# Optimization experiments

Measured on AMD Instinct MI355X. Metric: run time of the kernel, lower is better.

The kernel has to match this reference:

```python
import jax, jax.numpy as jnp
import numpy as np
from jax import lax

C, K, EMB = 10, 32, 32
B, H, W = 32, 128, 128
DIRS = ((-1, 0), (1, 0), (0, -1), (0, 1))  # up, down, left, right


def _shift(x, dh, dw):
    # shift (B,H,W,...) by (dh,dw) with zero fill; x[b,h,w] <- x[b,h+dh,w+dw]
    pad = [(0, 0), (max(dh, 0), max(-dh, 0)), (max(dw, 0), max(-dw, 0))] + [(0, 0)] * (x.ndim - 3)
    xp = jnp.pad(x, pad)
    h0, w0 = max(-dh, 0), max(-dw, 0)
    return lax.dynamic_slice_in_dim(lax.dynamic_slice_in_dim(xp, h0, x.shape[1], 1), w0, x.shape[2], 2)


def conv(x, w, b):
    y = lax.conv_general_dilated(x, w, (1, 1), 'SAME',
                                 dimension_numbers=('NHWC', 'HWIO', 'NHWC'))
    return y + b


def small_cnn(x, w1, b1, w2, b2, w3, b3):
    x = jax.nn.relu(conv(x, w1, b1))
    x = jax.nn.relu(conv(x, w2, b2))
    return conv(x, w3, b3)


def neighbor_affinity(phi, tau=0.5):
    # phi: (B,H,W,D) -> w: (B,H,W,4) Gaussian feature affinity to 4 neighbors
    ones = jnp.ones(phi.shape[:3] + (1,), phi.dtype)
    ws = []
    for dh, dw in DIRS:
        nb = _shift(phi, dh, dw)
        valid = _shift(ones, dh, dw)[..., 0]
        d2 = jnp.sum((phi - nb) ** 2, axis=-1)
        ws.append(jnp.exp(-d2 / tau) * valid)
    return jnp.stack(ws, axis=-1)


def init_seeds_soft(Bv, Hv, Wv, Kv, dtype=jnp.float32):
    # K seeds on a gh x gw grid; soft assignment by squared distance
    gh = 4
    gw = Kv // gh
    sh = (jnp.arange(gh, dtype=dtype) + 0.5) * (Hv / gh)
    sw = (jnp.arange(gw, dtype=dtype) + 0.5) * (Wv / gw)
    seed_h = jnp.repeat(sh, gw)  # (K,)
    seed_w = jnp.tile(sw, gh)    # (K,)
    hh = jnp.arange(Hv, dtype=dtype)[:, None, None]
    ww = jnp.arange(Wv, dtype=dtype)[None, :, None]
    d2 = (hh - seed_h) ** 2 + (ww - seed_w) ** 2  # (H,W,K)
    sigma2 = (Hv / gh) * (Wv / gw)
    A = jax.nn.softmax(-d2 / sigma2, axis=-1)
    return jnp.broadcast_to(A[None], (Bv, Hv, Wv, Kv))


def soft_message_pass(A, w, beta=2.0):
    # aggregate neighbor assignments weighted by affinity, renormalize over K
    agg = jnp.zeros_like(A)
    for d, (dh, dw) in enumerate(DIRS):
        agg = agg + w[..., d:d + 1] * _shift(A, dh, dw)
    return jax.nn.softmax(beta * agg, axis=-1)


def soft_pool_features(G, A):
    # G:(B,H,W,C), A:(B,H,W,K) -> T:(B,K,1+2+C+4)
    Bv, Hv, Wv, Cv = G.shape
    eps = 1e-6
    mass = jnp.sum(A, axis=(1, 2)) + eps                      # (B,K)
    hh = (jnp.arange(Hv, dtype=G.dtype) + 0.5) / Hv
    ww = (jnp.arange(Wv, dtype=G.dtype) + 0.5) / Wv
    h_c = jnp.einsum('bhwk,h->bk', A, hh) / mass
    w_c = jnp.einsum('bhwk,w->bk', A, ww) / mass
    col = jnp.einsum('bhwk,bhwc->bkc', A, G) / mass[..., None]
    h2 = jnp.einsum('bhwk,h->bk', A, hh ** 2) / mass
    w2 = jnp.einsum('bhwk,w->bk', A, ww ** 2) / mass
    h_sd = jnp.sqrt(jax.nn.relu(h2 - h_c ** 2) + eps)
    w_sd = jnp.sqrt(jax.nn.relu(w2 - w_c ** 2) + eps)
    size = (mass / (Hv * Wv))[..., None]                      # (B,K,1)
    cen = jnp.stack([h_c, w_c], axis=-1)                      # (B,K,2)
    bbox = jnp.stack([h_c - h_sd, h_c + h_sd, w_c - w_sd, w_c + w_sd], axis=-1)
    return jnp.concatenate([size, cen, col, bbox], axis=-1)


def setup_inputs() -> dict:
    key = jax.random.key(0)
    ks = jax.random.split(key, 4)
    X = jax.random.randint(ks[0], (B, H, W), 0, C)
    w1 = jax.random.normal(ks[1], (3, 3, C, 32), jnp.float32) * (1.0 / np.sqrt(9 * C))
    w2 = jax.random.normal(ks[2], (3, 3, 32, 32), jnp.float32) * (1.0 / np.sqrt(9 * 32))
    w3 = jax.random.normal(ks[3], (1, 1, 32, EMB), jnp.float32) * (1.0 / np.sqrt(32))
    return {'X': X, 'w1': w1, 'b1': jnp.zeros((32,), jnp.float32),
            'w2': w2, 'b2': jnp.zeros((32,), jnp.float32),
            'w3': w3, 'b3': jnp.zeros((EMB,), jnp.float32)}


def reference(X, w1, b1, w2, b2, w3, b3):
    G = jax.nn.one_hot(X, C, dtype=jnp.float32)              # (B,H,W,C)
    phi = small_cnn(G, w1, b1, w2, b2, w3, b3)               # (B,H,W,EMB)
    w = neighbor_affinity(phi)                               # (B,H,W,4)
    A = init_seeds_soft(G.shape[0], G.shape[1], G.shape[2], K, G.dtype)
    for _ in range(8):
        A = soft_message_pass(A, w, beta=2.0)
    T = soft_pool_features(G, A)
    return A, T
```

## Files before the change

### kernel.cpp

```cpp
#include <hip/hip_runtime.h>
#include <math.h>

#define HD 128
#define WD 128
#define BB 32
#define KK 32
#define NPIX (BB*HD*WD)
#define PLANE ((size_t)NPIX*8)

typedef _Float16 f16;
typedef __attribute__((ext_vector_type(8))) _Float16 f16x8;
typedef __attribute__((ext_vector_type(4))) _Float16 f16x4;
typedef __attribute__((ext_vector_type(4))) float f32x4;

__device__ __forceinline__ int swz(int row, int g){
  return row*64 + (((g + (row >> 1)) & 3) << 4);
}

__device__ __forceinline__ float xexp2(float x){
#if __has_builtin(__builtin_amdgcn_exp2f)
  return __builtin_amdgcn_exp2f(x);
#else
  return exp2f(x);
#endif
}
__device__ __forceinline__ float xrcp(float x){
#if __has_builtin(__builtin_amdgcn_rcpf)
  return __builtin_amdgcn_rcpf(x);
#else
  return 1.f/x;
#endif
}
__device__ __forceinline__ f16x8 bc8(f16 x){
  f16x8 v;
  #pragma unroll
  for (int j = 0; j < 8; j++) v[j] = x;
  return v;
}

#define WSCALE 2.8853900817779268f

__global__ __launch_bounds__(512, 2) void cnn_kernel(
    const int* __restrict__ X,
    const float* __restrict__ w1, const float* __restrict__ b1,
    const float* __restrict__ w2, const float* __restrict__ b2,
    const float* __restrict__ w3, const float* __restrict__ b3,
    f16* __restrict__ phi)
{
  __shared__ f16 sW1f[9*11*40];
  __shared__ int   sX[20*36];
  __shared__ float sB2[32], sB3[32];
  __shared__ f16 x1[612*32];
  __shared__ f16 w2t[9*32*32];
  __shared__ f16 w3t[32*32];

  const int tid = threadIdx.x;
  const int img = blockIdx.z;
  const int bh0 = blockIdx.y * 16;
  const int bw0 = blockIdx.x * 32;

  for (int i = tid; i < 9*11*32; i += 512) {
    int tap = i / 352, c = (i % 352) >> 5, oc = i & 31;
    float v = (c < 10) ? w1[tap*320 + c*32 + oc] : 0.f;
    if (tap == 4 && c < 10) v += b1[oc];
    sW1f[(tap*11 + c)*40 + oc] = (f16)v;
  }
  for (int i = tid; i < 9*32*32; i += 512) {
    int tap = i >> 10, ic = (i >> 5) & 31, oc = i & 31;
    int off = swz(tap*32 + oc, ic >> 3) + (ic & 7)*2;
    *(f16*)((char*)w2t + off) = (f16)w2[i];
  }
  for (int i = tid; i < 32*32; i += 512) {
    int ic = i >> 5, oe = i & 31;
    int off = swz(oe, ic >> 3) + (ic & 7)*2;
    *(f16*)((char*)w3t + off) = (f16)w3[i];
  }
  if (tid < 32) { sB2[tid] = b2[tid]; sB3[tid] = b3[tid]; }
  for (int i = tid; i < 20*36; i += 512) {
    int ti = i / 36, tj = i % 36;
    int gh = bh0 - 2 + ti, gw = bw0 - 2 + tj;
    sX[i] = (gh >= 0 && gh < HD && gw >= 0 && gw < WD) ? X[(img*HD + gh)*WD + gw] : 10;
  }
  __syncthreads();

  for (int p = tid; p < 612; p += 512) {
    int hr = p / 34, hc = p - hr*34;
    int gh = bh0 + hr - 1, gw = bw0 + hc - 1;
    if (gh >= 0 && gh < HD && gw >= 0 && gw < WD) {
      f16x8 acc[4];
      {
        int c = sX[hr*36 + hc];
        const f16* wr = &sW1f[c*40];
        #pragma unroll
        for (int g = 0; g < 4; g++) acc[g] = *(const f16x8*)(wr + g*8);
      }
      #pragma unroll
      for (int tap = 1; tap < 9; tap++) {
        const int ti = tap/3, tj = tap%3;
        int c = sX[(hr+ti)*36 + hc + tj];
        const f16* wr = &sW1f[(tap*11 + c)*40];
        #pragma unroll
        for (int g = 0; g < 4; g++) acc[g] += *(const f16x8*)(wr + g*8);
      }
      #pragma unroll
      for (int g = 0; g < 4; g++) {
        f16x8 r = acc[g];
        #pragma unroll
        for (int j = 0; j < 8; j++) r[j] = (r[j] > (f16)0.f) ? r[j] : (f16)0.f;
        *(f16x8*)((char*)x1 + swz(p, g)) = r;
      }
    } else {
      f16x8 z;
      #pragma unroll
      for (int j = 0; j < 8; j++) z[j] = (f16)0.f;
      #pragma unroll
      for (int g = 0; g < 4; g++) *(f16x8*)((char*)x1 + swz(p, g)) = z;
    }
  }
  __syncthreads();

  const int lane = tid & 63;
  const int wv   = tid >> 6;
  const int lr   = lane & 15;
  const int kg   = lane >> 4;
  const int mts  = wv * 4;

  int arow0[4];
  #pragma unroll
  for (int q = 0; q < 4; q++) {
    int px = (mts + q)*16 + lr;
    arow0[q] = (px >> 5)*34 + (px & 31);
  }
  float b2v0 = sB2[lr], b2v1 = sB2[lr + 16];
  f32x4 acc[4][2];
  #pragma unroll
  for (int q = 0; q < 4; q++) {
    acc[q][0] = (f32x4){b2v0, b2v0, b2v0, b2v0};
    acc[q][1] = (f32x4){b2v1, b2v1, b2v1, b2v1};
  }
  #pragma unroll
  for (int tap = 0; tap < 9; tap++) {
    const int ti = tap/3, tj = tap%3;
    f16x8 bf0 = *(const f16x8*)((const char*)w2t + swz(tap*32 + lr,      kg));
    f16x8 bf1 = *(const f16x8*)((const char*)w2t + swz(tap*32 + lr + 16, kg));
    #pragma unroll
    for (int q = 0; q < 4; q++) {
      int row = arow0[q] + ti*34 + tj;
      f16x8 af = *(const f16x8*)((const char*)x1 + swz(row, kg));
      acc[q][0] = __builtin_amdgcn_mfma_f32_16x16x32_f16(af, bf0, acc[q][0], 0, 0, 0);
      acc[q][1] = __builtin_amdgcn_mfma_f32_16x16x32_f16(af, bf1, acc[q][1], 0, 0, 0);
    }
  }
  __syncthreads();

  #pragma unroll
  for (int q = 0; q < 4; q++)
    #pragma unroll
    for (int nt = 0; nt < 2; nt++) {
      int oc = nt*16 + lr;
      #pragma unroll
      for (int rg = 0; rg < 4; rg++) {
        int px = (mts + q)*16 + kg*4 + rg;
        int off = swz(px, oc >> 3) + (oc & 7)*2;
        *(f16*)((char*)x1 + off) = (f16)fmaxf(acc[q][nt][rg], 0.f);
      }
    }
  __syncthreads();

  {
    f16x8 cf0 = *(const f16x8*)((const char*)w3t + swz(lr,      kg));
    f16x8 cf1 = *(const f16x8*)((const char*)w3t + swz(lr + 16, kg));
    float b3v0 = sB3[lr], b3v1 = sB3[lr + 16];
    #pragma unroll
    for (int q = 0; q < 4; q++) {
      f16x8 af = *(const f16x8*)((const char*)x1 + swz((mts + q)*16 + lr, kg));
      f32x4 o0 = (f32x4){b3v0, b3v0, b3v0, b3v0};
      f32x4 o1 = (f32x4){b3v1, b3v1, b3v1, b3v1};
      o0 = __builtin_amdgcn_mfma_f32_16x16x32_f16(af, cf0, o0, 0, 0, 0);
      o1 = __builtin_amdgcn_mfma_f32_16x16x32_f16(af, cf1, o1, 0, 0, 0);
      #pragma unroll
      for (int rg = 0; rg < 4; rg++) {
        int px = (mts + q)*16 + kg*4 + rg;
        int gh = bh0 + (px >> 5), gw = bw0 + (px & 31);
        f16* dst = phi + ((size_t)((img*HD + gh)*WD + gw))*32;
        dst[lr]      = (f16)o0[rg];
        dst[lr + 16] = (f16)o1[rg];
      }
    }
  }
}

__device__ __forceinline__ float aff_lds(const f16* __restrict__ sphi, int slot,
                                         f16x8 c0, f16x8 c1, f16x8 c2, f16x8 c3,
                                         bool valid) {
  f16x8 n0 = *(const f16x8*)((const char*)sphi + swz(slot, 0));
  f16x8 n1 = *(const f16x8*)((const char*)sphi + swz(slot, 1));
  f16x8 n2 = *(const f16x8*)((const char*)sphi + swz(slot, 2));
  f16x8 n3 = *(const f16x8*)((const char*)sphi + swz(slot, 3));
  f16x8 d0 = c0 - n0; f16x8 s = d0*d0;
  f16x8 d1 = c1 - n1; s += d1*d1;
  f16x8 d2 = c2 - n2; s += d2*d2;
  f16x8 d3 = c3 - n3; s += d3*d3;
  float d2f = 0.f;
  #pragma unroll
  for (int j = 0; j < 8; j++) d2f += (float)s[j];
  return valid ? WSCALE * xexp2(-WSCALE * d2f) : 0.f;
}

__global__ __launch_bounds__(256, 4) void aff_kernel(const f16* __restrict__ phi, float* __restrict__ wb) {
  __shared__ f16 sphi[612*32];

  const int blk  = blockIdx.x;
  const int tile = blk & 31;
  const int img  = blk >> 5;
  const int th0  = (tile >> 2) * 16;
  const int tw0  = (tile & 3) * 32;
  const size_t ibase = (size_t)img * HD * WD;

  for (int task = threadIdx.x; task < 2448; task += 256) {
    int p = task >> 2, g = task & 3;
    int r = p / 34, c = p - r*34;
    int gh = min(max(th0 - 1 + r, 0), HD-1);
    int gw = min(max(tw0 - 1 + c, 0), WD-1);
    f16x8 v = *(const f16x8*)(phi + (ibase + gh*WD + gw)*32 + g*8);
    *(f16x8*)((char*)sphi + swz(p, g)) = v;
  }
  __syncthreads();

  for (int p2 = threadIdx.x; p2 < 512; p2 += 256) {
    int r2 = p2 >> 5, c2 = p2 & 31;
    int gh = th0 + r2, gw = tw0 + c2;
    int qc = (r2+1)*34 + (c2+1);
    f16x8 c0 = *(const f16x8*)((const char*)sphi + swz(qc, 0));
    f16x8 c1 = *(const f16x8*)((const char*)sphi + swz(qc, 1));
    f16x8 c2v = *(const f16x8*)((const char*)sphi + swz(qc, 2));
    f16x8 c3 = *(const f16x8*)((const char*)sphi + swz(qc, 3));
    float4 out;
    out.x = aff_lds(sphi, qc + 34, c0,c1,c2v,c3, gh < HD-1);
    out.y = aff_lds(sphi, qc - 34, c0,c1,c2v,c3, gh > 0);
    out.z = aff_lds(sphi, qc + 1,  c0,c1,c2v,c3, gw < WD-1);
    out.w = aff_lds(sphi, qc - 1,  c0,c1,c2v,c3, gw > 0);
    ((float4*)wb)[ibase + gh*WD + gw] = out;
  }
}

__device__ __forceinline__ void a0_accum2(float* a, int hh, int ww, float wt) {
  const float C = 0.0028177637517362567f;
  float eh[4], ew[8];
  float sh = 0.f, sw = 0.f;
  const float fh = (float)hh, fw = (float)ww;
  #pragma unroll
  for (int kh = 0; kh < 4; kh++) { float d = fh - (float)(kh*32+16); eh[kh] = xexp2(-d*d*C); sh += eh[kh]; }
  #pragma unroll
  for (int kw = 0; kw < 8; kw++) { float d = fw - (float)(kw*16+8); ew[kw] = xexp2(-d*d*C); sw += ew[kw]; }
  float sc = wt * xrcp(sh * sw);
  #pragma unroll
  for (int kh = 0; kh < 4; kh++) {
    float ehs = eh[kh] * sc;
    #pragma unroll
    for (int kw = 0; kw < 8; kw++) a[kh*8+kw] = fmaf(ehs, ew[kw], a[kh*8+kw]);
  }
}

template<int FIRST>
__global__ __launch_bounds__(512, 6) void mp2_kernel(const f16* __restrict__ Ain,
                                                     const float* __restrict__ wb,
                                                     f16* __restrict__ Aout) {
  __shared__ f16 amid[612*32];

  const int blk  = blockIdx.x;
  const int xcd  = blk & 7;
  const int q    = blk >> 3;
  const int img  = xcd + ((q >> 5) << 3);
  const int tile = q & 31;
  const int th0  = (tile >> 2) * 16;
  const int tw0  = (tile & 3) * 32;
  const size_t ibase = (size_t)img * HD * WD;

  for (int p = threadIdx.x; p < 612; p += 512) {
    int r = p / 34, cc = p - r*34;
    int gh = th0 - 1 + r, gw = tw0 - 1 + cc;
    bool inimg = ((unsigned)gh < (unsigned)HD) && ((unsigned)gw < (unsigned)WD);
    int ghc = min(max(gh, 0), HD-1), gwc = min(max(gw, 0), WD-1);
    float4 wd = inimg ? ((const float4*)wb)[ibase + gh*WD + gw] : make_float4(0.f,0.f,0.f,0.f);
    int hu = ghc + ((ghc < HD-1) ? 1 : 0);
    int hd = ghc - ((ghc > 0)    ? 1 : 0);
    int wl = gwc + ((gwc < WD-1) ? 1 : 0);
    int wr = gwc - ((gwc > 0)    ? 1 : 0);

    float s = 0.f;
    f16x8 pe[4];
    if (FIRST) {
      float a[32];
      #pragma unroll
      for (int k = 0; k < 32; k++) a[k] = 0.f;
      a0_accum2(a, hu, gwc, wd.x);
      a0_accum2(a, hd, gwc, wd.y);
      a0_accum2(a, ghc, wl, wd.z);
      a0_accum2(a, ghc, wr, wd.w);
      #pragma unroll
      for (int g = 0; g < 4; g++)
        #pragma unroll
        for (int j = 0; j < 8; j++) { float e = xexp2(a[g*8+j]); s += e; pe[g][j] = (f16)e; }
    } else {
      const size_t iu_ = ibase + (size_t)hu*WD + gwc;
      const size_t id_ = ibase + (size_t)hd*WD + gwc;
      const size_t il_ = ibase + (size_t)ghc*WD + wl;
      const size_t ir_ = ibase + (size_t)ghc*WD + wr;
      f16x8 w0 = bc8((f16)wd.x), w1 = bc8((f16)wd.y), w2 = bc8((f16)wd.z), w3 = bc8((f16)wd.w);
      #pragma unroll
      for (int g = 0; g < 4; g++) {
        const f16* pg = Ain + (size_t)g*PLANE;
        f16x8 v0 = *(const f16x8*)(pg + iu_*8);
        f16x8 v1 = *(const f16x8*)(pg + id_*8);
        f16x8 v2 = *(const f16x8*)(pg + il_*8);
        f16x8 v3 = *(const f16x8*)(pg + ir_*8);
        f16x8 agg = v0*w0 + v1*w1 + v2*w2 + v3*w3;
        #pragma unroll
        for (int j = 0; j < 8; j++) { float e = xexp2((float)agg[j]); s += e; pe[g][j] = (f16)e; }
      }
    }
    f16x8 iv = bc8((f16)xrcp(s));
    #pragma unroll
    for (int g = 0; g < 4; g++)
      *(f16x8*)((char*)amid + swz(p, g)) = pe[g]*iv;
  }
  __syncthreads();

  {
    int r2 = threadIdx.x >> 5, c2 = threadIdx.x & 31;
    int gh = th0 + r2, gw = tw0 + c2;
    int rm = r2 + 1, cm = c2 + 1;
    float4 wd = ((const float4*)wb)[ibase + gh*WD + gw];
    int q0 = (rm + ((gh < HD-1) ? 1 : 0))*34 + cm;
    int q1 = (rm - ((gh > 0)    ? 1 : 0))*34 + cm;
    int q2 = rm*34 + cm + ((gw < WD-1) ? 1 : 0);
    int q3 = rm*34 + cm - ((gw > 0)    ? 1 : 0);
    f16x8 w0 = bc8((f16)wd.x), w1 = bc8((f16)wd.y), w2 = bc8((f16)wd.z), w3 = bc8((f16)wd.w);
    float s = 0.f;
    f16x8 pe[4];
    #pragma unroll
    for (int g = 0; g < 4; g++) {
      f16x8 v0 = *(const f16x8*)((const char*)amid + swz(q0, g));
      f16x8 v1 = *(const f16x8*)((const char*)amid + swz(q1, g));
      f16x8 v2 = *(const f16x8*)((const char*)amid + swz(q2, g));
      f16x8 v3 = *(const f16x8*)((const char*)amid + swz(q3, g));
      f16x8 agg = v0*w0 + v1*w1 + v2*w2 + v3*w3;
      #pragma unroll
      for (int j = 0; j < 8; j++) { float e = xexp2((float)agg[j]); s += e; pe[g][j] = (f16)e; }
    }
    f16x8 iv = bc8((f16)xrcp(s));
    size_t opix = ibase + (size_t)gh*WD + gw;
    #pragma unroll
    for (int g = 0; g < 4; g++)
      *(f16x8*)(Aout + (size_t)g*PLANE + opix*8) = pe[g]*iv;
  }
}

__global__ __launch_bounds__(512, 2) void mp2last_kernel(const f16* __restrict__ Ain,
                                                         const float* __restrict__ wb,
                                                         const int* __restrict__ X,
                                                         float* __restrict__ AoutF,
                                                         float* __restrict__ part) {
  __shared__ f16 amid[612*32];
  __shared__ float red[16*33*15];
  __shared__ int sXt[512];

  const int blk  = blockIdx.x;
  const int xcd  = blk & 7;
  const int q    = blk >> 3;
  const int img  = xcd + ((q >> 5) << 3);
  const int tile = q & 31;
  const int th0  = (tile >> 2) * 16;
  const int tw0  = (tile & 3) * 32;
  const size_t ibase = (size_t)img * HD * WD;

  {
    int r = threadIdx.x >> 5, c = threadIdx.x & 31;
    sXt[threadIdx.x] = X[ibase + (size_t)(th0 + r)*WD + tw0 + c];
  }

  for (int p = threadIdx.x; p < 612; p += 512) {
    int r = p / 34, cc = p - r*34;
    int gh = th0 - 1 + r, gw = tw0 - 1 + cc;
    bool inimg = ((unsigned)gh < (unsigned)HD) && ((unsigned)gw < (unsigned)WD);
    int ghc = min(max(gh, 0), HD-1), gwc = min(max(gw, 0), WD-1);
    float4 wd = inimg ? ((const float4*)wb)[ibase + gh*WD + gw] : make_float4(0.f,0.f,0.f,0.f);
    int hu = ghc + ((ghc < HD-1) ? 1 : 0);
    int hd = ghc - ((ghc > 0)    ? 1 : 0);
    int wl = gwc + ((gwc < WD-1) ? 1 : 0);
    int wr = gwc - ((gwc > 0)    ? 1 : 0);

    const size_t iu_ = ibase + (size_t)hu*WD + gwc;
    const size_t id_ = ibase + (size_t)hd*WD + gwc;
    const size_t il_ = ibase + (size_t)ghc*WD + wl;
    const size_t ir_ = ibase + (size_t)ghc*WD + wr;
    f16x8 w0 = bc8((f16)wd.x), w1 = bc8((f16)wd.y), w2 = bc8((f16)wd.z), w3 = bc8((f16)wd.w);
    float s = 0.f;
    f16x8 pe[4];
    #pragma unroll
    for (int g = 0; g < 4; g++) {
      const f16* pg = Ain + (size_t)g*PLANE;
      f16x8 v0 = *(const f16x8*)(pg + iu_*8);
      f16x8 v1 = *(const f16x8*)(pg + id_*8);
      f16x8 v2 = *(const f16x8*)(pg + il_*8);
      f16x8 v3 = *(const f16x8*)(pg + ir_*8);
      f16x8 agg = v0*w0 + v1*w1 + v2*w2 + v3*w3;
      #pragma unroll
      for (int j = 0; j < 8; j++) { float e = xexp2((float)agg[j]); s += e; pe[g][j] = (f16)e; }
    }
    f16x8 iv = bc8((f16)xrcp(s));
    #pragma unroll
    for (int g = 0; g < 4; g++)
      *(f16x8*)((char*)amid + swz(p, g)) = pe[g]*iv;
  }
  __syncthreads();

  f16x8 pe[4];
  {
    int r2 = threadIdx.x >> 5, c2 = threadIdx.x & 31;
    int gh = th0 + r2, gw = tw0 + c2;
    int rm = r2 + 1, cm = c2 + 1;
    float4 wd = ((const float4*)wb)[ibase + gh*WD + gw];
    int q0 = (rm + ((gh < HD-1) ? 1 : 0))*34 + cm;
    int q1 = (rm - ((gh > 0)    ? 1 : 0))*34 + cm;
    int q2 = rm*34 + cm + ((gw < WD-1) ? 1 : 0);
    int q3 = rm*34 + cm - ((gw > 0)    ? 1 : 0);
    f16x8 w0 = bc8((f16)wd.x), w1 = bc8((f16)wd.y), w2 = bc8((f16)wd.z), w3 = bc8((f16)wd.w);
    float s = 0.f;
    #pragma unroll
    for (int g = 0; g < 4; g++) {
      f16x8 v0 = *(const f16x8*)((const char*)amid + swz(q0, g));
      f16x8 v1 = *(const f16x8*)((const char*)amid + swz(q1, g));
      f16x8 v2 = *(const f16x8*)((const char*)amid + swz(q2, g));
      f16x8 v3 = *(const f16x8*)((const char*)amid + swz(q3, g));
      f16x8 agg = v0*w0 + v1*w1 + v2*w2 + v3*w3;
      #pragma unroll
      for (int j = 0; j < 8; j++) { float e = xexp2((float)agg[j]); s += e; pe[g][j] = (f16)e; }
    }
    f16x8 iv = bc8((f16)xrcp(s));
    #pragma unroll
    for (int g = 0; g < 4; g++) pe[g] = pe[g]*iv;
  }

  __syncthreads();
  f16* planes = amid;
  #pragma unroll
  for (int g = 0; g < 4; g++)
    *(f16x8*)((char*)planes + (g*513 + threadIdx.x)*16) = pe[g];
  __syncthreads();
  {
    float* obase = AoutF + ((size_t)(img*HD + th0)*WD + tw0)*32;
    #pragma unroll
    for (int rep = 0; rep < 8; rep++) {
      int flat = rep*512 + threadIdx.x;
      int row = flat >> 8;
      int within = flat & 255;
      int pxr = within >> 3;
      int kq = within & 7;
      int g = kq >> 1, half = kq & 1;
      int pxl = row*32 + pxr;
      f16x4 v = *(const f16x4*)((const char*)planes + (g*513 + pxl)*16 + half*8);
      float4 o;
      o.x = (float)v[0]; o.y = (float)v[1]; o.z = (float)v[2]; o.w = (float)v[3];
      *(float4*)(obase + (size_t)row*WD*32 + pxr*32 + kq*4) = o;
    }
  }

  {
    const int k  = threadIdx.x & 31;
    const int gr = threadIdx.x >> 5;
    const int gq = k >> 3, j = k & 7;
    const float hh = ((float)(th0 + gr) + 0.5f) * (1.f/128.f);
    float s0 = 0.f, sw = 0.f, sw2 = 0.f;
    float col[10];
    #pragma unroll
    for (int c = 0; c < 10; c++) col[c] = 0.f;
    #pragma unroll
    for (int i = 0; i < 32; i++) {
      int px = gr*32 + i;
      float a = (float)*(const f16*)((const char*)planes + (gq*513 + px)*16 + j*2);
      float ww = ((float)(tw0 + i) + 0.5f) * (1.f/128.f);
      s0 += a; sw = fmaf(ww, a, sw); sw2 = fmaf(ww*ww, a, sw2);
      int x = sXt[px];
      #pragma unroll
      for (int c = 0; c < 10; c++) col[c] += (x == c) ? a : 0.f;
    }
    float* rd = &red[(gr*33 + k)*15];
    rd[0] = s0; rd[1] = hh*s0; rd[2] = sw; rd[3] = hh*hh*s0; rd[4] = sw2;
    #pragma unroll
    for (int c = 0; c < 10; c++) rd[5+c] = col[c];
  }
  __syncthreads();
  if (threadIdx.x < 480) {
    int k = threadIdx.x / 15, qq = threadIdx.x - k*15;
    float v = 0.f;
    #pragma unroll
    for (int g = 0; g < 16; g++) v += red[(g*33 + k)*15 + qq];
    part[(((size_t)img*32 + tile)*32 + k)*15 + qq] = v;
  }
}

__global__ __launch_bounds__(256) void pool2_kernel(const float* __restrict__ part,
                                                    float* __restrict__ T) {
  const int t = blockIdx.x * 256 + threadIdx.x;
  if (t >= BB*KK) return;
  const int b = t >> 5, k = t & 31;
  float s[15];
  #pragma unroll
  for (int q = 0; q < 15; q++) s[q] = 0.f;
  for (int cy = 0; cy < 32; cy++) {
    const float* p = part + (((size_t)b*32 + cy)*32 + k)*15;
    #pragma unroll
    for (int q = 0; q < 15; q++) s[q] += p[q];
  }
  float mass = s[0] + 1e-6f;
  float inv  = 1.f / mass;
  float h_c = s[1]*inv, w_c = s[2]*inv, h2 = s[3]*inv, w2 = s[4]*inv;
  float h_sd = sqrtf(fmaxf(h2 - h_c*h_c, 0.f) + 1e-6f);
  float w_sd = sqrtf(fmaxf(w2 - w_c*w_c, 0.f) + 1e-6f);
  float* o = T + (size_t)t*17;
  o[0] = mass * (1.f/16384.f);
  o[1] = h_c; o[2] = w_c;
  #pragma unroll
  for (int c = 0; c < 10; c++) o[3+c] = s[5+c]*inv;
  o[13] = h_c - h_sd; o[14] = h_c + h_sd; o[15] = w_c - w_sd; o[16] = w_c + w_sd;
}

extern "C" void kernel_launch(void* const* d_in, const int* in_sizes, int n_in,
                              void* d_out, int out_size, void* d_ws, size_t ws_size,
                              hipStream_t stream) {
  const int*   X  = (const int*)d_in[0];
  const float* w1 = (const float*)d_in[1];
  const float* b1 = (const float*)d_in[2];
  const float* w2 = (const float*)d_in[3];
  const float* b2 = (const float*)d_in[4];
  const float* w3 = (const float*)d_in[5];
  const float* b3 = (const float*)d_in[6];

  float* out   = (float*)d_out;
  float* A_out = out;
  float* T_out = out + (size_t)NPIX * KK;

  char*  ws   = (char*)d_ws;
  f16*   bufA = (f16*)ws;
  f16*   bufB = (f16*)(ws + (size_t)32*1024*1024);
  float* wb   = (float*)(ws + (size_t)64*1024*1024);
  float* part = (float*)(ws + (size_t)72*1024*1024);

  f16* phi = bufB;
  cnn_kernel<<<dim3(WD/32, HD/16, BB), 512, 0, stream>>>(X, w1, b1, w2, b2, w3, b3, phi);
  aff_kernel<<<1024, 256, 0, stream>>>(phi, wb);

  mp2_kernel<1><<<1024, 512, 0, stream>>>(nullptr, wb, bufA);
  mp2_kernel<0><<<1024, 512, 0, stream>>>(bufA, wb, bufB);
  mp2_kernel<0><<<1024, 512, 0, stream>>>(bufB, wb, bufA);
  mp2last_kernel<<<1024, 512, 0, stream>>>(bufA, wb, X, A_out, part);

  pool2_kernel<<<(BB*KK + 255)/256, 256, 0, stream>>>(part, T_out);
}
```

Measured before the change: 234.2 us.

## Fuse affinity computation into first message-pass kernel with halo-extended phi tile

Merges aff_kernel and the FIRST mp2_kernel into one affmp2_kernel. It loads a 2-pixel halo of phi into LDS so affinities can be computed for the 1-pixel halo of the message-pass tile. The affinities are kept in LDS for the second step, and interior values are still written to global memory for later kernels. This removes one kernel launch and the round trip of writing and rereading wb. In exchange it recomputes affinities on halo pixels, uses more LDS, and drops occupancy to a launch bound of 2 blocks of 512 threads.

```diff
diff --git a/kernel.cpp b/kernel.cpp
--- a/kernel.cpp
+++ b/kernel.cpp
@@ -190,9 +190,28 @@
   }
 }
 
-__device__ __forceinline__ float aff_lds(const f16* __restrict__ sphi, int slot,
-                                         f16x8 c0, f16x8 c1, f16x8 c2, f16x8 c3,
-                                         bool valid) {
+__device__ __forceinline__ void a0_accum2(float* a, int hh, int ww, float wt) {
+  const float C = 0.0028177637517362567f;
+  float eh[4], ew[8];
+  float sh = 0.f, sw = 0.f;
+  const float fh = (float)hh, fw = (float)ww;
+  #pragma unroll
+  for (int kh = 0; kh < 4; kh++) { float d = fh - (float)(kh*32+16); eh[kh] = xexp2(-d*d*C); sh += eh[kh]; }
+  #pragma unroll
+  for (int kw = 0; kw < 8; kw++) { float d = fw - (float)(kw*16+8); ew[kw] = xexp2(-d*d*C); sw += ew[kw]; }
+  float sc = wt * xrcp(sh * sw);
+  #pragma unroll
+  for (int kh = 0; kh < 4; kh++) {
+    float ehs = eh[kh] * sc;
+    #pragma unroll
+    for (int kw = 0; kw < 8; kw++) a[kh*8+kw] = fmaf(ehs, ew[kw], a[kh*8+kw]);
+  }
+}
+
+__device__ __forceinline__ float aff36(const f16* __restrict__ sphi, int slot,
+                                       f16x8 c0, f16x8 c1, f16x8 c2, f16x8 c3,
+                                       bool valid) {
+  if (!valid) return 0.f;
   f16x8 n0 = *(const f16x8*)((const char*)sphi + swz(slot, 0));
   f16x8 n1 = *(const f16x8*)((const char*)sphi + swz(slot, 1));
   f16x8 n2 = *(const f16x8*)((const char*)sphi + swz(slot, 2));
@@ -204,65 +223,127 @@
   float d2f = 0.f;
   #pragma unroll
   for (int j = 0; j < 8; j++) d2f += (float)s[j];
-  return valid ? WSCALE * xexp2(-WSCALE * d2f) : 0.f;
-}
-
-__global__ __launch_bounds__(256, 4) void aff_kernel(const f16* __restrict__ phi, float* __restrict__ wb) {
-  __shared__ f16 sphi[612*32];
+  return WSCALE * xexp2(-WSCALE * d2f);
+}
+
+__global__ __launch_bounds__(512, 2) void affmp2_kernel(const f16* __restrict__ phi,
+                                                        float* __restrict__ wb,
+                                                        f16* __restrict__ Aout) {
+  __shared__ f16 sphi[720*32];
+  __shared__ float4 wbs[612];
 
   const int blk  = blockIdx.x;
-  const int tile = blk & 31;
-  const int img  = blk >> 5;
+  const int xcd  = blk & 7;
+  const int q    = blk >> 3;
+  const int img  = xcd + ((q >> 5) << 3);
+  const int tile = q & 31;
   const int th0  = (tile >> 2) * 16;
   const int tw0  = (tile & 3) * 32;
   const size_t ibase = (size_t)img * HD * WD;
 
-  for (int task = threadIdx.x; task < 2448; task += 256) {
+  for (int task = threadIdx.x; task < 2880; task += 512) {
     int p = task >> 2, g = task & 3;
-    int r = p / 34, c = p - r*34;
-    int gh = min(max(th0 - 1 + r, 0), HD-1);
-    int gw = min(max(tw0 - 1 + c, 0), WD-1);
-    f16x8 v = *(const f16x8*)(phi + (ibase + gh*WD + gw)*32 + g*8);
+    int r = p / 36, c = p - r*36;
+    int gh = min(max(th0 - 2 + r, 0), HD-1);
+    int gw = min(max(tw0 - 2 + c, 0), WD-1);
+    f16x8 v = *(const f16x8*)(phi + (ibase + (size_t)gh*WD + gw)*32 + g*8);
     *(f16x8*)((char*)sphi + swz(p, g)) = v;
   }
   __syncthreads();
 
-  for (int p2 = threadIdx.x; p2 < 512; p2 += 256) {
-    int r2 = p2 >> 5, c2 = p2 & 31;
+  f16x8 res0[4], res1[4];
+  const bool own1 = (threadIdx.x + 512) < 612;
+  #pragma unroll
+  for (int it = 0; it < 2; it++) {
+    if (it == 1 && !own1) break;
+    int p = threadIdx.x + it*512;
+    int r = p / 34, cc = p - r*34;
+    int gh = th0 - 1 + r, gw = tw0 - 1 + cc;
+    bool inimg = ((unsigned)gh < (unsigned)HD) && ((unsigned)gw < (unsigned)WD);
+    float4 wd = make_float4(0.f, 0.f, 0.f, 0.f);
+    if (inimg) {
+      int fs = (r + 1)*36 + (cc + 1);
+      f16x8 c0 = *(const f16x8*)((const char*)sphi + swz(fs, 0));
+      f16x8 c1 = *(const f16x8*)((const char*)sphi + swz(fs, 1));
+      f16x8 c2 = *(const f16x8*)((const char*)sphi + swz(fs, 2));
+      f16x8 c3 = *(const f16x8*)((const char*)sphi + swz(fs, 3));
+      wd.x = aff36(sphi, fs + 36, c0,c1,c2,c3, gh < HD-1);
+      wd.y = aff36(sphi, fs - 36, c0,c1,c2,c3, gh > 0);
+      wd.z = aff36(sphi, fs + 1,  c0,c1,c2,c3, gw < WD-1);
+      wd.w = aff36(sphi, fs - 1,  c0,c1,c2,c3, gw > 0);
+    }
+    wbs[p] = wd;
+    if (r >= 1 && r <= 16 && cc >= 1 && cc <= 32)
+      ((float4*)wb)[ibase + gh*WD + gw] = wd;
+
+    int ghc = min(max(gh, 0), HD-1), gwc = min(max(gw, 0), WD-1);
+    int hu = ghc + ((ghc < HD-1) ? 1 : 0);
+    int hd = ghc - ((ghc > 0)    ? 1 : 0);
+    int wl = gwc + ((gwc < WD-1) ? 1 : 0);
+    int wr = gwc - ((gwc > 0)    ? 1 : 0);
+    float a[32];
+    #pragma unroll
+    for (int k = 0; k < 32; k++) a[k] = 0.f;
+    a0_accum2(a, hu, gwc, wd.x);
+    a0_accum2(a, hd, gwc, wd.y);
+    a0_accum2(a, ghc, wl, wd.z);
+    a0_accum2(a, ghc, wr, wd.w);
+    float s = 0.f;
+    f16x8 pe[4];
+    #pragma unroll
+    for (int g = 0; g < 4; g++)
+      #pragma unroll
+      for (int j = 0; j < 8; j++) { float e = xexp2(a[g*8+j]); s += e; pe[g][j] = (f16)e; }
+    f16x8 iv = bc8((f16)xrcp(s));
+    #pragma unroll
+    for (int g = 0; g < 4; g++) {
+      if (it == 0) res0[g] = pe[g]*iv;
+      else         res1[g] = pe[g]*iv;
+    }
+  }
+  __syncthreads();
+
+  #pragma unroll
+  for (int g = 0; g < 4; g++)
+    *(f16x8*)((char*)sphi + swz(threadIdx.x, g)) = res0[g];
+  if (own1) {
+    #pragma unroll
+    for (int g = 0; g < 4; g++)
+      *(f16x8*)((char*)sphi + swz(threadIdx.x + 512, g)) = res1[g];
+  }
+  __syncthreads();
+
+  {
+    int r2 = threadIdx.x >> 5, c2 = threadIdx.x & 31;
     int gh = th0 + r2, gw = tw0 + c2;
-    int qc = (r2+1)*34 + (c2+1);
-    f16x8 c0 = *(const f16x8*)((const char*)sphi + swz(qc, 0));
-    f16x8 c1 = *(const f16x8*)((const char*)sphi + swz(qc, 1));
-    f16x8 c2v = *(const f16x8*)((const char*)sphi + swz(qc, 2));
-    f16x8 c3 = *(const f16x8*)((const char*)sphi + swz(qc, 3));
-    float4 out;
-    out.x = aff_lds(sphi, qc + 34, c0,c1,c2v,c3, gh < HD-1);
-    out.y = aff_lds(sphi, qc - 34, c0,c1,c2v,c3, gh > 0);
-    out.z = aff_lds(sphi, qc + 1,  c0,c1,c2v,c3, gw < WD-1);
-    out.w = aff_lds(sphi, qc - 1,  c0,c1,c2v,c3, gw > 0);
-    ((float4*)wb)[ibase + gh*WD + gw] = out;
-  }
-}
-
-__device__ __forceinline__ void a0_accum2(float* a, int hh, int ww, float wt) {
-  const float C = 0.0028177637517362567f;
-  float eh[4], ew[8];
-  float sh = 0.f, sw = 0.f;
-  const float fh = (float)hh, fw = (float)ww;
-  #pragma unroll
-  for (int kh = 0; kh < 4; kh++) { float d = fh - (float)(kh*32+16); eh[kh] = xexp2(-d*d*C); sh += eh[kh]; }
-  #pragma unroll
-  for (int kw = 0; kw < 8; kw++) { float d = fw - (float)(kw*16+8); ew[kw] = xexp2(-d*d*C); sw += ew[kw]; }
-  float sc = wt * xrcp(sh * sw);
-  #pragma unroll
-  for (int kh = 0; kh < 4; kh++) {
-    float ehs = eh[kh] * sc;
-    #pragma unroll
-    for (int kw = 0; kw < 8; kw++) a[kh*8+kw] = fmaf(ehs, ew[kw], a[kh*8+kw]);
-  }
-}
-
-template<int FIRST>
+    int rm = r2 + 1, cm = c2 + 1;
+    int pc_ = rm*34 + cm;
+    float4 wd = wbs[pc_];
+    int q0 = pc_ + ((gh < HD-1) ? 34 : 0);
+    int q1 = pc_ - ((gh > 0)    ? 34 : 0);
+    int q2 = pc_ + ((gw < WD-1) ? 1 : 0);
+    int q3 = pc_ - ((gw > 0)    ? 1 : 0);
+    f16x8 w0 = bc8((f16)wd.x), w1 = bc8((f16)wd.y), w2 = bc8((f16)wd.z), w3 = bc8((f16)wd.w);
+    float s = 0.f;
+    f16x8 pe[4];
+    #pragma unroll
+    for (int g = 0; g < 4; g++) {
+      f16x8 v0 = *(const f16x8*)((const char*)sphi + swz(q0, g));
+      f16x8 v1 = *(const f16x8*)((const char*)sphi + swz(q1, g));
+      f16x8 v2 = *(const f16x8*)((const char*)sphi + swz(q2, g));
+      f16x8 v3 = *(const f16x8*)((const char*)sphi + swz(q3, g));
+      f16x8 agg = v0*w0 + v1*w1 + v2*w2 + v3*w3;
+      #pragma unroll
+      for (int j = 0; j < 8; j++) { float e = xexp2((float)agg[j]); s += e; pe[g][j] = (f16)e; }
+    }
+    f16x8 iv = bc8((f16)xrcp(s));
+    size_t opix = ibase + (size_t)gh*WD + gw;
+    #pragma unroll
+    for (int g = 0; g < 4; g++)
+      *(f16x8*)(Aout + (size_t)g*PLANE + opix*8) = pe[g]*iv;
+  }
+}
+
 __global__ __launch_bounds__(512, 6) void mp2_kernel(const f16* __restrict__ Ain,
                                                      const float* __restrict__ wb,
                                                      f16* __restrict__ Aout) {
@@ -288,37 +369,23 @@
     int wl = gwc + ((gwc < WD-1) ? 1 : 0);
     int wr = gwc - ((gwc > 0)    ? 1 : 0);
 
+    const size_t iu_ = ibase + (size_t)hu*WD + gwc;
+    const size_t id_ = ibase + (size_t)hd*WD + gwc;
+    const size_t il_ = ibase + (size_t)ghc*WD + wl;
+    const size_t ir_ = ibase + (size_t)ghc*WD + wr;
+    f16x8 w0 = bc8((f16)wd.x), w1 = bc8((f16)wd.y), w2 = bc8((f16)wd.z), w3 = bc8((f16)wd.w);
     float s = 0.f;
     f16x8 pe[4];
-    if (FIRST) {
-      float a[32];
-      #pragma unroll
-      for (int k = 0; k < 32; k++) a[k] = 0.f;
-      a0_accum2(a, hu, gwc, wd.x);
-      a0_accum2(a, hd, gwc, wd.y);
-      a0_accum2(a, ghc, wl, wd.z);
-      a0_accum2(a, ghc, wr, wd.w);
-      #pragma unroll
-      for (int g = 0; g < 4; g++)
-        #pragma unroll
-        for (int j = 0; j < 8; j++) { float e = xexp2(a[g*8+j]); s += e; pe[g][j] = (f16)e; }
-    } else {
-      const size_t iu_ = ibase + (size_t)hu*WD + gwc;
-      const size_t id_ = ibase + (size_t)hd*WD + gwc;
-      const size_t il_ = ibase + (size_t)ghc*WD + wl;
-      const size_t ir_ = ibase + (size_t)ghc*WD + wr;
-      f16x8 w0 = bc8((f16)wd.x), w1 = bc8((f16)wd.y), w2 = bc8((f16)wd.z), w3 = bc8((f16)wd.w);
-      #pragma unroll
-      for (int g = 0; g < 4; g++) {
-        const f16* pg = Ain + (size_t)g*PLANE;
-        f16x8 v0 = *(const f16x8*)(pg + iu_*8);
-        f16x8 v1 = *(const f16x8*)(pg + id_*8);
-        f16x8 v2 = *(const f16x8*)(pg + il_*8);
-        f16x8 v3 = *(const f16x8*)(pg + ir_*8);
-        f16x8 agg = v0*w0 + v1*w1 + v2*w2 + v3*w3;
-        #pragma unroll
-        for (int j = 0; j < 8; j++) { float e = xexp2((float)agg[j]); s += e; pe[g][j] = (f16)e; }
-      }
+    #pragma unroll
+    for (int g = 0; g < 4; g++) {
+      const f16* pg = Ain + (size_t)g*PLANE;
+      f16x8 v0 = *(const f16x8*)(pg + iu_*8);
+      f16x8 v1 = *(const f16x8*)(pg + id_*8);
+      f16x8 v2 = *(const f16x8*)(pg + il_*8);
+      f16x8 v3 = *(const f16x8*)(pg + ir_*8);
+      f16x8 agg = v0*w0 + v1*w1 + v2*w2 + v3*w3;
+      #pragma unroll
+      for (int j = 0; j < 8; j++) { float e = xexp2((float)agg[j]); s += e; pe[g][j] = (f16)e; }
     }
     f16x8 iv = bc8((f16)xrcp(s));
     #pragma unroll
@@ -550,11 +617,10 @@
 
   f16* phi = bufB;
   cnn_kernel<<<dim3(WD/32, HD/16, BB), 512, 0, stream>>>(X, w1, b1, w2, b2, w3, b3, phi);
-  aff_kernel<<<1024, 256, 0, stream>>>(phi, wb);
-
-  mp2_kernel<1><<<1024, 512, 0, stream>>>(nullptr, wb, bufA);
-  mp2_kernel<0><<<1024, 512, 0, stream>>>(bufA, wb, bufB);
-  mp2_kernel<0><<<1024, 512, 0, stream>>>(bufB, wb, bufA);
+
+  affmp2_kernel<<<1024, 512, 0, stream>>>(phi, wb, bufA);
+  mp2_kernel<<<1024, 512, 0, stream>>>(bufA, wb, bufB);
+  mp2_kernel<<<1024, 512, 0, stream>>>(bufB, wb, bufA);
   mp2last_kernel<<<1024, 512, 0, stream>>>(bufA, wb, X, A_out, part);
 
   pool2_kernel<<<(BB*KK + 255)/256, 256, 0, stream>>>(part, T_out);
```

New measurement: 232.7 us. Within noise of the previous version (-0.7%).
